# Optimization experiments

Measured on AMD Instinct MI355X. Metric: run time of the kernel, lower is better.

Reference implementation:

```python
import jax, jax.numpy as jnp
import numpy as np

EPS = 1e-8  # torch F.cosine_similarity clamps each norm to eps

def setup_inputs() -> dict:
    key = jax.random.key(0)
    frames, height, width, hidden = 64, 23, 24, 1152
    total = frames * height * width  # 35328 image tokens
    hidden_states = jax.random.normal(key, (total, hidden), dtype=jnp.float32)
    return {
        "hidden_states": hidden_states,
        "frames": frames,
        "height": height,
        "width": width,
        "interval": 1,
    }

def _cos(a, b):
    dot = jnp.sum(a * b, axis=-1)
    na = jnp.maximum(jnp.linalg.norm(a, axis=-1), EPS)
    nb = jnp.maximum(jnp.linalg.norm(b, axis=-1), EPS)
    return dot / (na * nb)

def reference(hidden_states, frames, height, width, interval):
    # Faithful vectorized form of compute_token_similarities_vectorized:
    # for each frame f < frames-interval,
    #   right[f, i] = cos(x[f, i], x[f+interval, i+1])     for i in [0, tpf-2]
    #   down [f, i] = cos(x[f, i], x[f+interval, i+width]) for i in [0, tpf-width-1]
    # all other positions stay -1.
    tpf = height * width
    d = hidden_states.shape[-1]
    x = hidden_states.reshape(frames, tpf, d)
    valid = frames - interval

    right = _cos(x[:valid, : tpf - 1], x[interval:, 1:])            # [valid, tpf-1]
    down = _cos(x[:valid, : tpf - width], x[interval:, width:])      # [valid, tpf-width]

    right_full = jnp.full((frames, tpf), -1.0, dtype=hidden_states.dtype)
    right_full = right_full.at[:valid, : tpf - 1].set(right).reshape(-1)
    down_full = jnp.full((frames, tpf), -1.0, dtype=hidden_states.dtype)
    down_full = down_full.at[:valid, : tpf - width].set(down).reshape(-1)
    return right_full, down_full
```

## Files before the change

### kernel.cpp

```cpp
#include <hip/hip_runtime.h>
#include <math.h>

#define EPS 1e-8f

#define TPF   552
#define HID   1152
#define NTOK  35328
#define WID   24
#define NCHAINW 2898
#define NBLK  726


struct Row { float4 a, b, c, d; float2 e; };

__device__ __forceinline__ Row load_row(const float* __restrict__ p, int lane) {
    Row r;
    const float4* p4 = (const float4*)p;
    r.a = p4[lane];       r.b = p4[lane + 64];
    r.c = p4[lane + 128]; r.d = p4[lane + 192];
    r.e = ((const float2*)(p + 1024))[lane];
    return r;
}

__device__ __forceinline__ float dotrr(const Row& x, const Row& y) {
    float s = 0.f;
    s = fmaf(x.a.x, y.a.x, s); s = fmaf(x.a.y, y.a.y, s);
    s = fmaf(x.a.z, y.a.z, s); s = fmaf(x.a.w, y.a.w, s);
    s = fmaf(x.b.x, y.b.x, s); s = fmaf(x.b.y, y.b.y, s);
    s = fmaf(x.b.z, y.b.z, s); s = fmaf(x.b.w, y.b.w, s);
    s = fmaf(x.c.x, y.c.x, s); s = fmaf(x.c.y, y.c.y, s);
    s = fmaf(x.c.z, y.c.z, s); s = fmaf(x.c.w, y.c.w, s);
    s = fmaf(x.d.x, y.d.x, s); s = fmaf(x.d.y, y.d.y, s);
    s = fmaf(x.d.z, y.d.z, s); s = fmaf(x.d.w, y.d.w, s);
    s = fmaf(x.e.x, y.e.x, s); s = fmaf(x.e.y, y.e.y, s);
    return s;
}

__device__ __forceinline__ float reduce64(float v) {
    #pragma unroll
    for (int m = 1; m < 64; m <<= 1) v += __shfl_xor(v, m, 64);
    return v;
}

__global__ void __launch_bounds__(256) simdiff_chain_kernel(
    const float* __restrict__ x,
    const int* __restrict__ p_frames,
    const int* __restrict__ p_width,
    const int* __restrict__ p_interval,
    float* __restrict__ out)
{
    const int frames   = *p_frames;
    const int width    = *p_width;
    const int interval = *p_interval;
    const int lane     = threadIdx.x & 63;
    const int w        = blockIdx.x * (blockDim.x >> 6) + (threadIdx.x >> 6);

    const bool spec = (frames == 64) && (width == WID) && (interval == 1);

    if (spec) {
        if (w >= NCHAINW) {
            for (int i = (w - NCHAINW) * 64 + lane; i < 2 * TPF; i += 6 * 64) {
                if (i < TPF) out[63 * TPF + i]          = -1.f;
                else         out[NTOK + 63 * TPF + (i - TPF)] = -1.f;
            }
            return;
        }
        const int seg    = w & 1;
        const int chain  = w >> 1;
        const int f      = chain / 23;
        const int c0     = chain - f * 23;
        const int cstart = c0 + 276 * seg;

        const float* xf  = x + (size_t)(f * TPF) * HID;
        const float* xf1 = x + (size_t)((f + 1) * TPF) * HID;

        Row bcur = load_row(xf1 + (size_t)(cstart + 1)  * HID, lane);
        Row bnxt = load_row(xf1 + (size_t)(cstart + 24) * HID, lane);
        Row acur = load_row(xf  + (size_t)cstart        * HID, lane);
        float nbcur = reduce64(dotrr(bcur, bcur));

        #pragma unroll
        for (int j = 0; j < 12; ++j) {
            const int c = cstart + 23 * j;

            Row anxt = {}; Row bn2 = {};
            if (j < 11) {
                anxt = load_row(xf + (size_t)(c + 23) * HID, lane);
                const int b2col = c + 47;
                if (b2col < TPF)
                    bn2 = load_row(xf1 + (size_t)b2col * HID, lane);
            }

            float na    = reduce64(dotrr(acur, acur));
            float d1    = reduce64(dotrr(acur, bcur));
            float d2    = reduce64(dotrr(acur, bnxt));
            float nbnxt = reduce64(dotrr(bnxt, bnxt));

            if (lane == 0) {
                const int t  = f * TPF + c;
                const float sa = fmaxf(sqrtf(na), EPS);
                out[t]        = (c < TPF - 1)
                    ? d1 / (sa * fmaxf(sqrtf(nbcur), EPS)) : -1.f;
                out[NTOK + t] = (c < TPF - WID)
                    ? d2 / (sa * fmaxf(sqrtf(nbnxt), EPS)) : -1.f;
            }
            nbcur = nbnxt; acur = anxt; bcur = bnxt; bnxt = bn2;
        }
        return;
    }

    const int ntok    = NTOK;
    const int tpf     = ntok / frames;
    const int valid_f = frames - interval;
    const int stride  = gridDim.x * (blockDim.x >> 6);
    for (int task = w; task < ntok; task += stride) {
        const int f = task / tpf;
        const int i = task - f * tpf;
        const bool rv = (f < valid_f) && (i < tpf - 1);
        const bool dv = (f < valid_f) && (i < tpf - width);
        float out_r = -1.f, out_d = -1.f;
        if (rv || dv) {
            const float* A  = x + (size_t)task * HID;
            const float* B1 = rv ? x + (size_t)((f + interval) * tpf + i + 1) * HID : A;
            const float* B2 = dv ? x + (size_t)((f + interval) * tpf + i + width) * HID : A;
            Row a = load_row(A, lane), b1 = load_row(B1, lane), b2 = load_row(B2, lane);
            float na  = reduce64(dotrr(a, a));
            float nb1 = reduce64(dotrr(b1, b1));
            float nb2 = reduce64(dotrr(b2, b2));
            float d1  = reduce64(dotrr(a, b1));
            float d2  = reduce64(dotrr(a, b2));
            const float sa = fmaxf(sqrtf(na), EPS);
            if (rv) out_r = d1 / (sa * fmaxf(sqrtf(nb1), EPS));
            if (dv) out_d = d2 / (sa * fmaxf(sqrtf(nb2), EPS));
        }
        if (lane == 0) {
            out[task]        = out_r;
            out[ntok + task] = out_d;
        }
    }
}

__global__ void __launch_bounds__(256) simdiff_generic_kernel(
    const float* __restrict__ x,
    const int* __restrict__ p_frames,
    const int* __restrict__ p_width,
    const int* __restrict__ p_interval,
    float* __restrict__ out,
    int ntok, int hidden)
{
    const int frames   = *p_frames;
    const int width    = *p_width;
    const int interval = *p_interval;
    const int tpf      = ntok / frames;
    const int valid_f  = frames - interval;
    const int lane     = threadIdx.x & 63;
    const int stride   = gridDim.x * (blockDim.x >> 6);
    const int nvec     = hidden >> 2;

    for (int task = blockIdx.x * (blockDim.x >> 6) + (threadIdx.x >> 6);
         task < ntok; task += stride) {
        const int f = task / tpf;
        const int i = task - f * tpf;
        const bool rv = (f < valid_f) && (i < tpf - 1);
        const bool dv = (f < valid_f) && (i < tpf - width);
        float out_r = -1.f, out_d = -1.f;
        if (rv || dv) {
            const float4* A  = (const float4*)(x + (size_t)task * hidden);
            const float4* B1 = rv ? (const float4*)(x + (size_t)((f + interval) * tpf + i + 1) * hidden) : A;
            const float4* B2 = dv ? (const float4*)(x + (size_t)((f + interval) * tpf + i + width) * hidden) : A;
            float na2 = 0.f, nb1 = 0.f, nb2 = 0.f, d1 = 0.f, d2 = 0.f;
            for (int v = lane; v < nvec; v += 64) {
                const float4 a = A[v];
                na2 = fmaf(a.x,a.x, fmaf(a.y,a.y, fmaf(a.z,a.z, fmaf(a.w,a.w, na2))));
                const float4 b = B1[v];
                nb1 = fmaf(b.x,b.x, fmaf(b.y,b.y, fmaf(b.z,b.z, fmaf(b.w,b.w, nb1))));
                d1  = fmaf(a.x,b.x, fmaf(a.y,b.y, fmaf(a.z,b.z, fmaf(a.w,b.w, d1))));
                const float4 cc = B2[v];
                nb2 = fmaf(cc.x,cc.x, fmaf(cc.y,cc.y, fmaf(cc.z,cc.z, fmaf(cc.w,cc.w, nb2))));
                d2  = fmaf(a.x,cc.x, fmaf(a.y,cc.y, fmaf(a.z,cc.z, fmaf(a.w,cc.w, d2))));
            }
            #pragma unroll
            for (int m = 1; m < 64; m <<= 1) {
                na2 += __shfl_xor(na2, m, 64);
                nb1 += __shfl_xor(nb1, m, 64);
                nb2 += __shfl_xor(nb2, m, 64);
                d1  += __shfl_xor(d1, m, 64);
                d2  += __shfl_xor(d2, m, 64);
            }
            const float sa = fmaxf(sqrtf(na2), EPS);
            if (rv) out_r = d1 / (sa * fmaxf(sqrtf(nb1), EPS));
            if (dv) out_d = d2 / (sa * fmaxf(sqrtf(nb2), EPS));
        }
        if (lane == 0) {
            out[task]        = out_r;
            out[ntok + task] = out_d;
        }
    }
}

extern "C" void kernel_launch(void* const* d_in, const int* in_sizes, int n_in,
                              void* d_out, int out_size, void* d_ws, size_t ws_size,
                              hipStream_t stream) {
    const float* x        = (const float*)d_in[0];
    const int* p_frames   = (const int*)d_in[1];
    const int* p_width    = (const int*)d_in[3];
    const int* p_interval = (const int*)d_in[4];
    float* out            = (float*)d_out;

    const int ntok   = out_size / 2;
    const int hidden = in_sizes[0] / ntok;

    if (ntok == NTOK && hidden == HID) {
        simdiff_chain_kernel<<<NBLK, 256, 0, stream>>>(
            x, p_frames, p_width, p_interval, out);
    } else {
        const int blocks = (ntok + 3) / 4;
        simdiff_generic_kernel<<<blocks, 256, 0, stream>>>(
            x, p_frames, p_width, p_interval, out, ntok, hidden);
    }
}
```

Baseline: 235.9 us.

## Replace long per-wave chains with two-token pair tasks for more parallelism

```diff
diff --git a/kernel.cpp b/kernel.cpp
--- a/kernel.cpp
+++ b/kernel.cpp
@@ -7,9 +7,12 @@
 #define HID   1152
 #define NTOK  35328
 #define WID   24
-#define NCHAINW 2898
-#define NBLK  726
-
+
+#define PAIRS_PER_FRAME 276
+#define NPAIRW  17388
+#define NFILLW  20
+#define NWAVES  17408
+#define NBLK    4352
 
 struct Row { float4 a, b, c, d; float2 e; };
 
@@ -42,7 +45,7 @@
     return v;
 }
 
-__global__ void __launch_bounds__(256) simdiff_chain_kernel(
+__global__ void __launch_bounds__(256) simdiff_pair_kernel(
     const float* __restrict__ x,
     const int* __restrict__ p_frames,
     const int* __restrict__ p_width,
@@ -58,53 +61,61 @@
     const bool spec = (frames == 64) && (width == WID) && (interval == 1);
 
     if (spec) {
-        if (w >= NCHAINW) {
-            for (int i = (w - NCHAINW) * 64 + lane; i < 2 * TPF; i += 6 * 64) {
-                if (i < TPF) out[63 * TPF + i]          = -1.f;
+        if (w >= NPAIRW) {
+            for (int i = (w - NPAIRW) * 64 + lane; i < 2 * TPF; i += NFILLW * 64) {
+                if (i < TPF) out[63 * TPF + i]                = -1.f;
                 else         out[NTOK + 63 * TPF + (i - TPF)] = -1.f;
             }
             return;
         }
-        const int seg    = w & 1;
-        const int chain  = w >> 1;
-        const int f      = chain / 23;
-        const int c0     = chain - f * 23;
-        const int cstart = c0 + 276 * seg;
+        const int f    = w / PAIRS_PER_FRAME;
+        const int p    = w - f * PAIRS_PER_FRAME;
+        const int k    = p / 23;
+        const int j    = p - k * 23;
+        const int c1   = 46 * k + j;
+        const int c2   = c1 + 23;
+
+        const bool dv1 = (c1 < TPF - WID);
+        const bool rv2 = (c2 < TPF - 1);
+        const bool dv2 = (c2 < TPF - WID);
 
         const float* xf  = x + (size_t)(f * TPF) * HID;
         const float* xf1 = x + (size_t)((f + 1) * TPF) * HID;
 
-        Row bcur = load_row(xf1 + (size_t)(cstart + 1)  * HID, lane);
-        Row bnxt = load_row(xf1 + (size_t)(cstart + 24) * HID, lane);
-        Row acur = load_row(xf  + (size_t)cstart        * HID, lane);
-        float nbcur = reduce64(dotrr(bcur, bcur));
-
-        #pragma unroll
-        for (int j = 0; j < 12; ++j) {
-            const int c = cstart + 23 * j;
-
-            Row anxt = {}; Row bn2 = {};
-            if (j < 11) {
-                anxt = load_row(xf + (size_t)(c + 23) * HID, lane);
-                const int b2col = c + 47;
-                if (b2col < TPF)
-                    bn2 = load_row(xf1 + (size_t)b2col * HID, lane);
-            }
-
-            float na    = reduce64(dotrr(acur, acur));
-            float d1    = reduce64(dotrr(acur, bcur));
-            float d2    = reduce64(dotrr(acur, bnxt));
-            float nbnxt = reduce64(dotrr(bnxt, bnxt));
-
-            if (lane == 0) {
-                const int t  = f * TPF + c;
-                const float sa = fmaxf(sqrtf(na), EPS);
-                out[t]        = (c < TPF - 1)
-                    ? d1 / (sa * fmaxf(sqrtf(nbcur), EPS)) : -1.f;
-                out[NTOK + t] = (c < TPF - WID)
-                    ? d2 / (sa * fmaxf(sqrtf(nbnxt), EPS)) : -1.f;
-            }
-            nbcur = nbnxt; acur = anxt; bcur = bnxt; bnxt = bn2;
+        const float* pA1 = xf  + (size_t)c1 * HID;
+        const float* pA2 = xf  + (size_t)c2 * HID;
+        const float* pB1 = xf1 + (size_t)(c1 + 1) * HID;
+        const float* pBs = (dv1 || rv2) ? xf1 + (size_t)(c1 + WID) * HID : pA1;
+        const float* pB3 = dv2          ? xf1 + (size_t)(c2 + WID) * HID : pA1;
+
+        const Row A1 = load_row(pA1, lane);
+        const Row A2 = load_row(pA2, lane);
+        const Row B1 = load_row(pB1, lane);
+        const Row Bs = load_row(pBs, lane);
+        const Row B3 = load_row(pB3, lane);
+
+        float na1 = reduce64(dotrr(A1, A1));
+        float na2 = reduce64(dotrr(A2, A2));
+        float nb1 = reduce64(dotrr(B1, B1));
+        float nbs = reduce64(dotrr(Bs, Bs));
+        float nb3 = reduce64(dotrr(B3, B3));
+        float d11 = reduce64(dotrr(A1, B1));
+        float d1s = reduce64(dotrr(A1, Bs));
+        float d2s = reduce64(dotrr(A2, Bs));
+        float d23 = reduce64(dotrr(A2, B3));
+
+        if (lane == 0) {
+            const int t1 = f * TPF + c1;
+            const int t2 = f * TPF + c2;
+            const float sa1 = fmaxf(sqrtf(na1), EPS);
+            const float sa2 = fmaxf(sqrtf(na2), EPS);
+            const float sb1 = fmaxf(sqrtf(nb1), EPS);
+            const float sbs = fmaxf(sqrtf(nbs), EPS);
+            const float sb3 = fmaxf(sqrtf(nb3), EPS);
+            out[t1]        = d11 / (sa1 * sb1);
+            out[NTOK + t1] = dv1 ? d1s / (sa1 * sbs) : -1.f;
+            out[t2]        = rv2 ? d2s / (sa2 * sbs) : -1.f;
+            out[NTOK + t2] = dv2 ? d23 / (sa2 * sb3) : -1.f;
         }
         return;
     }
@@ -211,7 +222,7 @@
     const int hidden = in_sizes[0] / ntok;
 
     if (ntok == NTOK && hidden == HID) {
-        simdiff_chain_kernel<<<NBLK, 256, 0, stream>>>(
+        simdiff_pair_kernel<<<NBLK, 256, 0, stream>>>(
             x, p_frames, p_width, p_interval, out);
     } else {
         const int blocks = (ntok + 3) / 4;
```

Result: no change. 232.2 us (-1.6%).
